# Optimization experiments

Hardware: AMD Instinct MI355X
Metric: run time of the kernel (lower is better)

## Reference

```python
import jax, jax.numpy as jnp
import numpy as np

N_EMBD = 1568  # 2 * 784, hard-coded in the source module
HEAD_SIZE = 128
BATCH = 16384


def setup_inputs() -> dict:
    key = jax.random.key(0)
    kx, kq, kk, kv = jax.random.split(key, 4)
    x = jax.random.normal(kx, (BATCH, N_EMBD), dtype=jnp.float32)
    wq = jax.random.normal(kq, (N_EMBD, HEAD_SIZE), dtype=jnp.float32) * (N_EMBD ** -0.5)
    wk = jax.random.normal(kk, (N_EMBD, HEAD_SIZE), dtype=jnp.float32) * (N_EMBD ** -0.5)
    wv = jax.random.normal(kv, (N_EMBD, HEAD_SIZE), dtype=jnp.float32) * (N_EMBD ** -0.5)
    return {"x": x, "wq": wq, "wk": wk, "wv": wv}


def reference(x, wq, wk, wv):
    # x: [B, N]; projections (bias-free Linear): [B, H]
    B, N = x.shape
    q = x @ wq
    k = x @ wk
    v = x @ wv
    # Outer-product score matrix per batch element: [B, H, H]
    attn = jnp.einsum('bi,bj->bij', q, k) * (N ** -0.5)  # scale uses FEATURE dim N, as in source
    attn = jax.nn.softmax(attn, axis=-1)
    # dropout is identity in eval mode
    out = jnp.einsum('bij,bj->bi', attn, v)  # [B, H]
    return out
```

## Files before the change

### kernel.cpp

```cpp
#include <hip/hip_runtime.h>
#include <stdint.h>

typedef unsigned short u16;
typedef __bf16 bf16x8 __attribute__((ext_vector_type(8)));
typedef float f32x4 __attribute__((ext_vector_type(4)));
typedef float f32x2 __attribute__((ext_vector_type(2)));

#define M_ROWS 16384
#define K_DIM  1568
#define H_DIM  128
#define NQ     384
#define MT     64
#define BK     32
#define NSTEP  49
#define NCH    8
#define CH_F   192
#define ASTR   200
#define TSTR   40
#define ABUF   (MT * ASTR)
#define PSTR   132
#define KSTRIDE (NQ * BK)
#define SCALE  0.02525381361380526f
#define LOG2E  1.4426950408889634f

__device__ __forceinline__ u16 f32_to_bf16_rne(float f) {
    uint32_t u = __float_as_uint(f);
    uint32_t r = (u + 0x7FFFu + ((u >> 16) & 1u)) >> 16;
    return (u16)r;
}

__device__ __forceinline__ uint32_t cvt_pk(float lo, float hi) {
    uint32_t d;
    asm("v_cvt_pk_bf16_f32 %0, %1, %2" : "=v"(d) : "v"(lo), "v"(hi));
    return d;
}

__device__ __forceinline__ f32x2 pk_mul(f32x2 a, f32x2 b) {
    f32x2 d; asm("v_pk_mul_f32 %0, %1, %2" : "=v"(d) : "v"(a), "v"(b)); return d;
}
__device__ __forceinline__ f32x2 pk_add(f32x2 a, f32x2 b) {
    f32x2 d; asm("v_pk_add_f32 %0, %1, %2" : "=v"(d) : "v"(a), "v"(b)); return d;
}
__device__ __forceinline__ f32x2 pk_fma(f32x2 a, f32x2 b, f32x2 c) {
    f32x2 d; asm("v_pk_fma_f32 %0, %1, %2, %3" : "=v"(d) : "v"(a), "v"(b), "v"(c)); return d;
}

__device__ __forceinline__ void cvt_wr8(u16* dst, f32x4 v) {
    uint2 t; t.x = cvt_pk(v.x, v.y); t.y = cvt_pk(v.z, v.w);
    *(uint2*)dst = t;
}

#define MFMA(a, b, c) __builtin_amdgcn_mfma_f32_16x16x32_bf16(a, b, c, 0, 0, 0)

__global__ __launch_bounds__(256) void wtrans_kernel(
    const float* __restrict__ wq, const float* __restrict__ wk,
    const float* __restrict__ wv, u16* __restrict__ wt2)
{
    __shared__ u16 tile[32][33];
    const float* w = (blockIdx.z == 0) ? wq : (blockIdx.z == 1) ? wk : wv;
    const int k0 = blockIdx.x * 32;
    const int nloc0 = blockIdx.y * 32;
    const int ng0 = blockIdx.z * 128 + nloc0;

    const int tn = threadIdx.x & 31;
    const int tk = threadIdx.x >> 5;
    #pragma unroll
    for (int p = 0; p < 4; p++) {
        int kk = tk + p * 8;
        tile[kk][tn] = f32_to_bf16_rne(w[(size_t)(k0 + kk) * H_DIM + nloc0 + tn]);
    }
    __syncthreads();

    const int klo = threadIdx.x & 31;
    const int tn2 = threadIdx.x >> 5;
    u16* dst = wt2 + (size_t)(k0 >> 5) * KSTRIDE;
    #pragma unroll
    for (int p = 0; p < 4; p++) {
        int nn = tn2 + p * 8;
        dst[(size_t)(ng0 + nn) * 32 + klo] = tile[klo][nn];
    }
}

__global__ __launch_bounds__(512, 2) void fused_kernel(
    const float* __restrict__ x,
    const u16* __restrict__ wt2,
    float* __restrict__ out)
{
    __shared__ char smem[3 * MT * PSTR * 4];
    u16* A0 = (u16*)smem;
    u16* A1 = A0 + ABUF;
    u16* TB = A1 + ABUF;
    float (*Pq)[PSTR] = (float (*)[PSTR])smem;
    float (*Pk)[PSTR] = (float (*)[PSTR])(smem + MT * PSTR * 4);
    float (*Pv)[PSTR] = (float (*)[PSTR])(smem + 2 * MT * PSTR * 4);

    const int tid  = threadIdx.x;
    const int lane = tid & 63;
    const int wave = tid >> 6;
    const int lrow = lane & 15;
    const int quad = lane >> 4;
    const int m0   = blockIdx.x * MT;

    const u16* bp0 = wt2 + (size_t)(wave * 48 +  0 + lrow) * 32 + quad * 8;
    const u16* bp1 = wt2 + (size_t)(wave * 48 + 16 + lrow) * 32 + quad * 8;
    const u16* bp2 = wt2 + (size_t)(wave * 48 + 32 + lrow) * 32 + quad * 8;

    const int srow = tid >> 3;
    const int st8  = tid & 7;
    const float* xrow = x + (size_t)(m0 + srow) * K_DIM;
    u16* wbs[2];
    wbs[0] = A0 + srow * ASTR + st8 * 4;
    wbs[1] = A1 + srow * ASTR + st8 * 4;

    const u16* aF[2][4];
    #pragma unroll
    for (int m = 0; m < 4; m++) {
        aF[0][m] = A0 + (m * 16 + lrow) * ASTR + quad * 8;
        aF[1][m] = A1 + (m * 16 + lrow) * ASTR + quad * 8;
    }

#define NTLD4(off) __builtin_nontemporal_load((const f32x4*)(xrow + (off)))
#define LOADC(S, OFF) do { \
    S[0] = NTLD4((OFF) + st8 * 4 +   0); \
    S[1] = NTLD4((OFF) + st8 * 4 +  32); \
    S[2] = NTLD4((OFF) + st8 * 4 +  64); \
    S[3] = NTLD4((OFF) + st8 * 4 +  96); \
    S[4] = NTLD4((OFF) + st8 * 4 + 128); \
    S[5] = NTLD4((OFF) + st8 * 4 + 160); \
} while (0)
#define WRITEC(WB, S) do { \
    cvt_wr8((WB) +   0, S[0]); cvt_wr8((WB) +  32, S[1]); \
    cvt_wr8((WB) +  64, S[2]); cvt_wr8((WB) +  96, S[3]); \
    cvt_wr8((WB) + 128, S[4]); cvt_wr8((WB) + 160, S[5]); \
} while (0)

    f32x4 acc00 = {}, acc01 = {}, acc02 = {};
    f32x4 acc10 = {}, acc11 = {}, acc12 = {};
    f32x4 acc20 = {}, acc21 = {}, acc22 = {};
    f32x4 acc30 = {}, acc31 = {}, acc32 = {};
    f32x4 sreg[2][6];

    LOADC(sreg[0], 0);
    f32x4 tl = NTLD4(1536 + st8 * 4);
    LOADC(sreg[1], CH_F);
    WRITEC(wbs[0], sreg[0]);
    cvt_wr8(TB + srow * TSTR + st8 * 4, tl);

    bf16x8 Ba0 = *(const bf16x8*)(bp0);
    bf16x8 Ba1 = *(const bf16x8*)(bp1);
    bf16x8 Ba2 = *(const bf16x8*)(bp2);
    bf16x8 Bb0 = *(const bf16x8*)(bp0 + KSTRIDE);
    bf16x8 Bb1 = *(const bf16x8*)(bp1 + KSTRIDE);
    bf16x8 Bb2 = *(const bf16x8*)(bp2 + KSTRIDE);
    __syncthreads();

#define KSTEP(AP, IT, G) do { \
    int gp = (G) + 2; if (gp > NSTEP - 1) gp = NSTEP - 1; \
    const size_t o = (size_t)gp * KSTRIDE; \
    bf16x8 Bc0 = *(const bf16x8*)(bp0 + o); \
    bf16x8 Bc1 = *(const bf16x8*)(bp1 + o); \
    bf16x8 Bc2 = *(const bf16x8*)(bp2 + o); \
    bf16x8 a0 = *(const bf16x8*)((AP)[0] + (IT) * BK); \
    bf16x8 a1 = *(const bf16x8*)((AP)[1] + (IT) * BK); \
    bf16x8 a2 = *(const bf16x8*)((AP)[2] + (IT) * BK); \
    bf16x8 a3 = *(const bf16x8*)((AP)[3] + (IT) * BK); \
    acc00 = MFMA(a0, Ba0, acc00); acc10 = MFMA(a1, Ba0, acc10); \
    acc20 = MFMA(a2, Ba0, acc20); acc30 = MFMA(a3, Ba0, acc30); \
    acc01 = MFMA(a0, Ba1, acc01); acc11 = MFMA(a1, Ba1, acc11); \
    acc21 = MFMA(a2, Ba1, acc21); acc31 = MFMA(a3, Ba1, acc31); \
    acc02 = MFMA(a0, Ba2, acc02); acc12 = MFMA(a1, Ba2, acc12); \
    acc22 = MFMA(a2, Ba2, acc22); acc32 = MFMA(a3, Ba2, acc32); \
    Ba0 = Bb0; Ba1 = Bb1; Ba2 = Bb2; Bb0 = Bc0; Bb1 = Bc1; Bb2 = Bc2; \
} while (0)

    #pragma unroll
    for (int c = 0; c < NCH; ++c) {
        if (c < NCH - 1) WRITEC(wbs[(c + 1) & 1], sreg[(c + 1) & 1]);
        if (c < NCH - 2) LOADC(sreg[c & 1], (c + 2) * CH_F);
        #pragma unroll
        for (int it = 0; it < 6; ++it) KSTEP(aF[c & 1], it, c * 6 + it);
        __syncthreads();
    }

    {
        bf16x8 a0 = *(const bf16x8*)(TB + (lrow +  0) * TSTR + quad * 8);
        bf16x8 a1 = *(const bf16x8*)(TB + (lrow + 16) * TSTR + quad * 8);
        bf16x8 a2 = *(const bf16x8*)(TB + (lrow + 32) * TSTR + quad * 8);
        bf16x8 a3 = *(const bf16x8*)(TB + (lrow + 48) * TSTR + quad * 8);
        acc00 = MFMA(a0, Ba0, acc00); acc10 = MFMA(a1, Ba0, acc10);
        acc20 = MFMA(a2, Ba0, acc20); acc30 = MFMA(a3, Ba0, acc30);
        acc01 = MFMA(a0, Ba1, acc01); acc11 = MFMA(a1, Ba1, acc11);
        acc21 = MFMA(a2, Ba1, acc21); acc31 = MFMA(a3, Ba1, acc31);
        acc02 = MFMA(a0, Ba2, acc02); acc12 = MFMA(a1, Ba2, acc12);
        acc22 = MFMA(a2, Ba2, acc22); acc32 = MFMA(a3, Ba2, acc32);
    }
    __syncthreads();

#define SCAT(ACC, MTi, NTi) do { \
    const int base = wave * 48 + (NTi) * 16; \
    const int sel  = base >> 7; \
    const int col  = (base & 127) + lrow; \
    const int mrow = (MTi) * 16 + quad * 4; \
    if (sel == 0)      { _Pragma("unroll") for (int rr = 0; rr < 4; rr++) Pq[mrow + rr][col] = ACC[rr] * (SCALE * LOG2E); } \
    else if (sel == 1) { _Pragma("unroll") for (int rr = 0; rr < 4; rr++) Pk[mrow + rr][col] = ACC[rr]; } \
    else               { _Pragma("unroll") for (int rr = 0; rr < 4; rr++) Pv[mrow + rr][col] = ACC[rr]; } \
} while (0)

    SCAT(acc00, 0, 0); SCAT(acc01, 0, 1); SCAT(acc02, 0, 2);
    SCAT(acc10, 1, 0); SCAT(acc11, 1, 1); SCAT(acc12, 1, 2);
    SCAT(acc20, 2, 0); SCAT(acc21, 2, 1); SCAT(acc22, 2, 2);
    SCAT(acc30, 3, 0); SCAT(acc31, 3, 1); SCAT(acc32, 3, 2);
    __syncthreads();

    const int r   = tid >> 3;
    const int sub = tid & 7;

    f32x4 qa = *(const f32x4*)&Pq[r][sub * 16 +  0];
    f32x4 qb = *(const f32x4*)&Pq[r][sub * 16 +  4];
    f32x4 qc = *(const f32x4*)&Pq[r][sub * 16 +  8];
    f32x4 qd = *(const f32x4*)&Pq[r][sub * 16 + 12];
    f32x2 qp0; qp0.x = qa.x; qp0.y = qa.y;
    f32x2 qp1; qp1.x = qa.z; qp1.y = qa.w;
    f32x2 qp2; qp2.x = qb.x; qp2.y = qb.y;
    f32x2 qp3; qp3.x = qb.z; qp3.y = qb.w;
    f32x2 qp4; qp4.x = qc.x; qp4.y = qc.y;
    f32x2 qp5; qp5.x = qc.z; qp5.y = qc.w;
    f32x2 qp6; qp6.x = qd.x; qp6.y = qd.y;
    f32x2 qp7; qp7.x = qd.z; qp7.y = qd.w;

    f32x2 d0 = {}, d1 = {}, d2 = {}, d3 = {}, d4 = {}, d5 = {}, d6 = {}, d7 = {};
    f32x2 n0 = {}, n1 = {}, n2 = {}, n3 = {}, n4 = {}, n5 = {}, n6 = {}, n7 = {};

    #pragma unroll 2
    for (int j4 = 0; j4 < 32; ++j4) {
        f32x4 k4 = *(const f32x4*)&Pk[r][j4 * 4];
        f32x4 v4 = *(const f32x4*)&Pv[r][j4 * 4];
        #pragma unroll
        for (int jj = 0; jj < 4; ++jj) {
            float kj = k4[jj];
            float vj = v4[jj];
            f32x2 kk; kk.x = kj; kk.y = kj;
            f32x2 vv; vv.x = vj; vv.y = vj;
            f32x2 s0 = pk_mul(qp0, kk);
            f32x2 s1 = pk_mul(qp1, kk);
            f32x2 s2 = pk_mul(qp2, kk);
            f32x2 s3 = pk_mul(qp3, kk);
            f32x2 s4 = pk_mul(qp4, kk);
            f32x2 s5 = pk_mul(qp5, kk);
            f32x2 s6 = pk_mul(qp6, kk);
            f32x2 s7 = pk_mul(qp7, kk);
            f32x2 e0; e0.x = __builtin_amdgcn_exp2f(s0.x); e0.y = __builtin_amdgcn_exp2f(s0.y);
            f32x2 e1; e1.x = __builtin_amdgcn_exp2f(s1.x); e1.y = __builtin_amdgcn_exp2f(s1.y);
            f32x2 e2; e2.x = __builtin_amdgcn_exp2f(s2.x); e2.y = __builtin_amdgcn_exp2f(s2.y);
            f32x2 e3; e3.x = __builtin_amdgcn_exp2f(s3.x); e3.y = __builtin_amdgcn_exp2f(s3.y);
            f32x2 e4; e4.x = __builtin_amdgcn_exp2f(s4.x); e4.y = __builtin_amdgcn_exp2f(s4.y);
            f32x2 e5; e5.x = __builtin_amdgcn_exp2f(s5.x); e5.y = __builtin_amdgcn_exp2f(s5.y);
            f32x2 e6; e6.x = __builtin_amdgcn_exp2f(s6.x); e6.y = __builtin_amdgcn_exp2f(s6.y);
            f32x2 e7; e7.x = __builtin_amdgcn_exp2f(s7.x); e7.y = __builtin_amdgcn_exp2f(s7.y);
            d0 = pk_add(d0, e0); n0 = pk_fma(e0, vv, n0);
            d1 = pk_add(d1, e1); n1 = pk_fma(e1, vv, n1);
            d2 = pk_add(d2, e2); n2 = pk_fma(e2, vv, n2);
            d3 = pk_add(d3, e3); n3 = pk_fma(e3, vv, n3);
            d4 = pk_add(d4, e4); n4 = pk_fma(e4, vv, n4);
            d5 = pk_add(d5, e5); n5 = pk_fma(e5, vv, n5);
            d6 = pk_add(d6, e6); n6 = pk_fma(e6, vv, n6);
            d7 = pk_add(d7, e7); n7 = pk_fma(e7, vv, n7);
        }
    }

    float* op = out + (size_t)(m0 + r) * H_DIM + sub * 16;
    f32x4 o0, o1, o2, o3;
    o0.x = n0.x / d0.x; o0.y = n0.y / d0.y; o0.z = n1.x / d1.x; o0.w = n1.y / d1.y;
    o1.x = n2.x / d2.x; o1.y = n2.y / d2.y; o1.z = n3.x / d3.x; o1.w = n3.y / d3.y;
    o2.x = n4.x / d4.x; o2.y = n4.y / d4.y; o2.z = n5.x / d5.x; o2.w = n5.y / d5.y;
    o3.x = n6.x / d6.x; o3.y = n6.y / d6.y; o3.z = n7.x / d7.x; o3.w = n7.y / d7.y;
    __builtin_nontemporal_store(o0, (f32x4*)(op +  0));
    __builtin_nontemporal_store(o1, (f32x4*)(op +  4));
    __builtin_nontemporal_store(o2, (f32x4*)(op +  8));
    __builtin_nontemporal_store(o3, (f32x4*)(op + 12));
}

extern "C" void kernel_launch(void* const* d_in, const int* in_sizes, int n_in,
                              void* d_out, int out_size, void* d_ws, size_t ws_size,
                              hipStream_t stream)
{
    const float* x  = (const float*)d_in[0];
    const float* wq = (const float*)d_in[1];
    const float* wk = (const float*)d_in[2];
    const float* wv = (const float*)d_in[3];
    float* out = (float*)d_out;

    u16* wt2 = (u16*)d_ws;

    wtrans_kernel<<<dim3(K_DIM / 32, H_DIM / 32, 3), 256, 0, stream>>>(wq, wk, wv, wt2);
    fused_kernel<<<M_ROWS / MT, 512, 0, stream>>>(x, wt2, out);
}
```

Measured before the change: 195.9 us.

## Split fused projection+attention into separate GEMM and attention kernels via workspace

When the workspace is large enough, the fused kernel is replaced by a projection kernel that writes scaled Q/K/V (fp32) to global memory, followed by a separate attention kernel that does the per-row outer-product softmax with 16 rows per 256-thread block. The aim is to lift the LDS footprint and occupancy limit that the fused epilogue imposes on the GEMM, and to spread the attention work over more threads. In exchange it adds a 25 MB write and read of the projection buffer and an extra launch. The old fused path is kept as a fallback.

Result: slower. 207.6 us (+6.0%).

```diff
diff --git a/kernel.cpp b/kernel.cpp
--- a/kernel.cpp
+++ b/kernel.cpp
@@ -23,6 +23,8 @@
 #define SCALE  0.02525381361380526f
 #define LOG2E  1.4426950408889634f
 
+#define WS_NEEDED ((size_t)M_ROWS * NQ * 4 + (size_t)NSTEP * KSTRIDE * 2)
+
 __device__ __forceinline__ u16 f32_to_bf16_rne(float f) {
     uint32_t u = __float_as_uint(f);
     uint32_t r = (u + 0x7FFFu + ((u >> 16) & 1u)) >> 16;
@@ -81,42 +83,27 @@
     }
 }
 
-__global__ __launch_bounds__(512, 2) void fused_kernel(
-    const float* __restrict__ x,
-    const u16* __restrict__ wt2,
-    float* __restrict__ out)
-{
-    __shared__ char smem[3 * MT * PSTR * 4];
-    u16* A0 = (u16*)smem;
-    u16* A1 = A0 + ABUF;
-    u16* TB = A1 + ABUF;
-    float (*Pq)[PSTR] = (float (*)[PSTR])smem;
-    float (*Pk)[PSTR] = (float (*)[PSTR])(smem + MT * PSTR * 4);
-    float (*Pv)[PSTR] = (float (*)[PSTR])(smem + 2 * MT * PSTR * 4);
-
-    const int tid  = threadIdx.x;
-    const int lane = tid & 63;
-    const int wave = tid >> 6;
-    const int lrow = lane & 15;
-    const int quad = lane >> 4;
-    const int m0   = blockIdx.x * MT;
-
-    const u16* bp0 = wt2 + (size_t)(wave * 48 +  0 + lrow) * 32 + quad * 8;
-    const u16* bp1 = wt2 + (size_t)(wave * 48 + 16 + lrow) * 32 + quad * 8;
-    const u16* bp2 = wt2 + (size_t)(wave * 48 + 32 + lrow) * 32 + quad * 8;
-
-    const int srow = tid >> 3;
-    const int st8  = tid & 7;
-    const float* xrow = x + (size_t)(m0 + srow) * K_DIM;
-    u16* wbs[2];
-    wbs[0] = A0 + srow * ASTR + st8 * 4;
-    wbs[1] = A1 + srow * ASTR + st8 * 4;
-
-    const u16* aF[2][4];
-    #pragma unroll
-    for (int m = 0; m < 4; m++) {
-        aF[0][m] = A0 + (m * 16 + lrow) * ASTR + quad * 8;
-        aF[1][m] = A1 + (m * 16 + lrow) * ASTR + quad * 8;
+#define GEMM_BODY_DECLS \
+    const int tid  = threadIdx.x; \
+    const int lane = tid & 63; \
+    const int wave = tid >> 6; \
+    const int lrow = lane & 15; \
+    const int quad = lane >> 4; \
+    const int m0   = blockIdx.x * MT; \
+    const u16* bp0 = wt2 + (size_t)(wave * 48 +  0 + lrow) * 32 + quad * 8; \
+    const u16* bp1 = wt2 + (size_t)(wave * 48 + 16 + lrow) * 32 + quad * 8; \
+    const u16* bp2 = wt2 + (size_t)(wave * 48 + 32 + lrow) * 32 + quad * 8; \
+    const int srow = tid >> 3; \
+    const int st8  = tid & 7; \
+    const float* xrow = x + (size_t)(m0 + srow) * K_DIM; \
+    u16* wbs[2]; \
+    wbs[0] = A0 + srow * ASTR + st8 * 4; \
+    wbs[1] = A1 + srow * ASTR + st8 * 4; \
+    const u16* aF[2][4]; \
+    _Pragma("unroll") \
+    for (int m = 0; m < 4; m++) { \
+        aF[0][m] = A0 + (m * 16 + lrow) * ASTR + quad * 8; \
+        aF[1][m] = A1 + (m * 16 + lrow) * ASTR + quad * 8; \
     }
 
 #define NTLD4(off) __builtin_nontemporal_load((const f32x4*)(xrow + (off)))
@@ -133,26 +120,6 @@
     cvt_wr8((WB) +  64, S[2]); cvt_wr8((WB) +  96, S[3]); \
     cvt_wr8((WB) + 128, S[4]); cvt_wr8((WB) + 160, S[5]); \
 } while (0)
-
-    f32x4 acc00 = {}, acc01 = {}, acc02 = {};
-    f32x4 acc10 = {}, acc11 = {}, acc12 = {};
-    f32x4 acc20 = {}, acc21 = {}, acc22 = {};
-    f32x4 acc30 = {}, acc31 = {}, acc32 = {};
-    f32x4 sreg[2][6];
-
-    LOADC(sreg[0], 0);
-    f32x4 tl = NTLD4(1536 + st8 * 4);
-    LOADC(sreg[1], CH_F);
-    WRITEC(wbs[0], sreg[0]);
-    cvt_wr8(TB + srow * TSTR + st8 * 4, tl);
-
-    bf16x8 Ba0 = *(const bf16x8*)(bp0);
-    bf16x8 Ba1 = *(const bf16x8*)(bp1);
-    bf16x8 Ba2 = *(const bf16x8*)(bp2);
-    bf16x8 Bb0 = *(const bf16x8*)(bp0 + KSTRIDE);
-    bf16x8 Bb1 = *(const bf16x8*)(bp1 + KSTRIDE);
-    bf16x8 Bb2 = *(const bf16x8*)(bp2 + KSTRIDE);
-    __syncthreads();
 
 #define KSTEP(AP, IT, G) do { \
     int gp = (G) + 2; if (gp > NSTEP - 1) gp = NSTEP - 1; \
@@ -173,27 +140,85 @@
     Ba0 = Bb0; Ba1 = Bb1; Ba2 = Bb2; Bb0 = Bc0; Bb1 = Bc1; Bb2 = Bc2; \
 } while (0)
 
-    #pragma unroll
-    for (int c = 0; c < NCH; ++c) {
-        if (c < NCH - 1) WRITEC(wbs[(c + 1) & 1], sreg[(c + 1) & 1]);
-        if (c < NCH - 2) LOADC(sreg[c & 1], (c + 2) * CH_F);
-        #pragma unroll
-        for (int it = 0; it < 6; ++it) KSTEP(aF[c & 1], it, c * 6 + it);
-        __syncthreads();
-    }
-
-    {
-        bf16x8 a0 = *(const bf16x8*)(TB + (lrow +  0) * TSTR + quad * 8);
-        bf16x8 a1 = *(const bf16x8*)(TB + (lrow + 16) * TSTR + quad * 8);
-        bf16x8 a2 = *(const bf16x8*)(TB + (lrow + 32) * TSTR + quad * 8);
-        bf16x8 a3 = *(const bf16x8*)(TB + (lrow + 48) * TSTR + quad * 8);
-        acc00 = MFMA(a0, Ba0, acc00); acc10 = MFMA(a1, Ba0, acc10);
-        acc20 = MFMA(a2, Ba0, acc20); acc30 = MFMA(a3, Ba0, acc30);
-        acc01 = MFMA(a0, Ba1, acc01); acc11 = MFMA(a1, Ba1, acc11);
-        acc21 = MFMA(a2, Ba1, acc21); acc31 = MFMA(a3, Ba1, acc31);
-        acc02 = MFMA(a0, Ba2, acc02); acc12 = MFMA(a1, Ba2, acc12);
-        acc22 = MFMA(a2, Ba2, acc22); acc32 = MFMA(a3, Ba2, acc32);
-    }
+#define GEMM_MAIN \
+    f32x4 acc00 = {}, acc01 = {}, acc02 = {}; \
+    f32x4 acc10 = {}, acc11 = {}, acc12 = {}; \
+    f32x4 acc20 = {}, acc21 = {}, acc22 = {}; \
+    f32x4 acc30 = {}, acc31 = {}, acc32 = {}; \
+    f32x4 sreg[2][6]; \
+    LOADC(sreg[0], 0); \
+    f32x4 tl = NTLD4(1536 + st8 * 4); \
+    LOADC(sreg[1], CH_F); \
+    WRITEC(wbs[0], sreg[0]); \
+    cvt_wr8(TB + srow * TSTR + st8 * 4, tl); \
+    bf16x8 Ba0 = *(const bf16x8*)(bp0); \
+    bf16x8 Ba1 = *(const bf16x8*)(bp1); \
+    bf16x8 Ba2 = *(const bf16x8*)(bp2); \
+    bf16x8 Bb0 = *(const bf16x8*)(bp0 + KSTRIDE); \
+    bf16x8 Bb1 = *(const bf16x8*)(bp1 + KSTRIDE); \
+    bf16x8 Bb2 = *(const bf16x8*)(bp2 + KSTRIDE); \
+    __syncthreads(); \
+    _Pragma("unroll") \
+    for (int c = 0; c < NCH; ++c) { \
+        if (c < NCH - 1) WRITEC(wbs[(c + 1) & 1], sreg[(c + 1) & 1]); \
+        if (c < NCH - 2) LOADC(sreg[c & 1], (c + 2) * CH_F); \
+        _Pragma("unroll") \
+        for (int it = 0; it < 6; ++it) KSTEP(aF[c & 1], it, c * 6 + it); \
+        __syncthreads(); \
+    } \
+    { \
+        bf16x8 a0 = *(const bf16x8*)(TB + (lrow +  0) * TSTR + quad * 8); \
+        bf16x8 a1 = *(const bf16x8*)(TB + (lrow + 16) * TSTR + quad * 8); \
+        bf16x8 a2 = *(const bf16x8*)(TB + (lrow + 32) * TSTR + quad * 8); \
+        bf16x8 a3 = *(const bf16x8*)(TB + (lrow + 48) * TSTR + quad * 8); \
+        acc00 = MFMA(a0, Ba0, acc00); acc10 = MFMA(a1, Ba0, acc10); \
+        acc20 = MFMA(a2, Ba0, acc20); acc30 = MFMA(a3, Ba0, acc30); \
+        acc01 = MFMA(a0, Ba1, acc01); acc11 = MFMA(a1, Ba1, acc11); \
+        acc21 = MFMA(a2, Ba1, acc21); acc31 = MFMA(a3, Ba1, acc31); \
+        acc02 = MFMA(a0, Ba2, acc02); acc12 = MFMA(a1, Ba2, acc12); \
+        acc22 = MFMA(a2, Ba2, acc22); acc32 = MFMA(a3, Ba2, acc32); \
+    }
+
+__global__ __launch_bounds__(512, 2) void proj_kernel(
+    const float* __restrict__ x, const u16* __restrict__ wt2,
+    float* __restrict__ P)
+{
+    __shared__ char smem[2 * ABUF * 2 + MT * TSTR * 2];
+    u16* A0 = (u16*)smem;
+    u16* A1 = A0 + ABUF;
+    u16* TB = A1 + ABUF;
+
+    GEMM_BODY_DECLS
+    GEMM_MAIN
+
+#define SCATG(ACC, MTi, NTi) do { \
+    const int n   = wave * 48 + (NTi) * 16 + lrow; \
+    const float sc = (n < 128) ? (SCALE * LOG2E) : 1.0f; \
+    const int mrow = m0 + (MTi) * 16 + quad * 4; \
+    _Pragma("unroll") for (int rr = 0; rr < 4; rr++) \
+        __builtin_nontemporal_store(ACC[rr] * sc, &P[(size_t)(mrow + rr) * NQ + n]); \
+} while (0)
+
+    SCATG(acc00, 0, 0); SCATG(acc01, 0, 1); SCATG(acc02, 0, 2);
+    SCATG(acc10, 1, 0); SCATG(acc11, 1, 1); SCATG(acc12, 1, 2);
+    SCATG(acc20, 2, 0); SCATG(acc21, 2, 1); SCATG(acc22, 2, 2);
+    SCATG(acc30, 3, 0); SCATG(acc31, 3, 1); SCATG(acc32, 3, 2);
+}
+
+__global__ __launch_bounds__(512, 2) void fused_kernel(
+    const float* __restrict__ x, const u16* __restrict__ wt2,
+    float* __restrict__ out)
+{
+    __shared__ char smem[3 * MT * PSTR * 4];
+    u16* A0 = (u16*)smem;
+    u16* A1 = A0 + ABUF;
+    u16* TB = A1 + ABUF;
+    float (*Pq)[PSTR] = (float (*)[PSTR])smem;
+    float (*Pk)[PSTR] = (float (*)[PSTR])(smem + MT * PSTR * 4);
+    float (*Pv)[PSTR] = (float (*)[PSTR])(smem + 2 * MT * PSTR * 4);
+
+    GEMM_BODY_DECLS
+    GEMM_MAIN
     __syncthreads();
 
 #define SCAT(ACC, MTi, NTi) do { \
@@ -280,6 +305,59 @@
     __builtin_nontemporal_store(o3, (f32x4*)(op + 12));
 }
 
+__global__ __launch_bounds__(256) void attn_kernel(
+    const float* __restrict__ P,
+    float* __restrict__ out)
+{
+    const int tid  = threadIdx.x;
+    const int rloc = tid >> 4;
+    const int sub  = tid & 15;
+    const int row  = blockIdx.x * 16 + rloc;
+    const float* pr = P + (size_t)row * NQ;
+
+    f32x4 qa = *(const f32x4*)(pr + sub * 8);
+    f32x4 qb = *(const f32x4*)(pr + sub * 8 + 4);
+    f32x2 qp0; qp0.x = qa.x; qp0.y = qa.y;
+    f32x2 qp1; qp1.x = qa.z; qp1.y = qa.w;
+    f32x2 qp2; qp2.x = qb.x; qp2.y = qb.y;
+    f32x2 qp3; qp3.x = qb.z; qp3.y = qb.w;
+
+    f32x2 d0 = {}, d1 = {}, d2 = {}, d3 = {};
+    f32x2 n0 = {}, n1 = {}, n2 = {}, n3 = {};
+
+    #pragma unroll 4
+    for (int j4 = 0; j4 < 32; ++j4) {
+        f32x4 k4 = *(const f32x4*)(pr + 128 + j4 * 4);
+        f32x4 v4 = *(const f32x4*)(pr + 256 + j4 * 4);
+        #pragma unroll
+        for (int jj = 0; jj < 4; ++jj) {
+            float kj = k4[jj];
+            float vj = v4[jj];
+            f32x2 kk; kk.x = kj; kk.y = kj;
+            f32x2 vv; vv.x = vj; vv.y = vj;
+            f32x2 s0 = pk_mul(qp0, kk);
+            f32x2 s1 = pk_mul(qp1, kk);
+            f32x2 s2 = pk_mul(qp2, kk);
+            f32x2 s3 = pk_mul(qp3, kk);
+            f32x2 e0; e0.x = __builtin_amdgcn_exp2f(s0.x); e0.y = __builtin_amdgcn_exp2f(s0.y);
+            f32x2 e1; e1.x = __builtin_amdgcn_exp2f(s1.x); e1.y = __builtin_amdgcn_exp2f(s1.y);
+            f32x2 e2; e2.x = __builtin_amdgcn_exp2f(s2.x); e2.y = __builtin_amdgcn_exp2f(s2.y);
+            f32x2 e3; e3.x = __builtin_amdgcn_exp2f(s3.x); e3.y = __builtin_amdgcn_exp2f(s3.y);
+            d0 = pk_add(d0, e0); n0 = pk_fma(e0, vv, n0);
+            d1 = pk_add(d1, e1); n1 = pk_fma(e1, vv, n1);
+            d2 = pk_add(d2, e2); n2 = pk_fma(e2, vv, n2);
+            d3 = pk_add(d3, e3); n3 = pk_fma(e3, vv, n3);
+        }
+    }
+
+    float* op = out + (size_t)row * H_DIM + sub * 8;
+    f32x4 o0, o1;
+    o0.x = n0.x / d0.x; o0.y = n0.y / d0.y; o0.z = n1.x / d1.x; o0.w = n1.y / d1.y;
+    o1.x = n2.x / d2.x; o1.y = n2.y / d2.y; o1.z = n3.x / d3.x; o1.w = n3.y / d3.y;
+    __builtin_nontemporal_store(o0, (f32x4*)(op));
+    __builtin_nontemporal_store(o1, (f32x4*)(op + 4));
+}
+
 extern "C" void kernel_launch(void* const* d_in, const int* in_sizes, int n_in,
                               void* d_out, int out_size, void* d_ws, size_t ws_size,
                               hipStream_t stream)
@@ -290,8 +368,15 @@
     const float* wv = (const float*)d_in[3];
     float* out = (float*)d_out;
 
-    u16* wt2 = (u16*)d_ws;
-
-    wtrans_kernel<<<dim3(K_DIM / 32, H_DIM / 32, 3), 256, 0, stream>>>(wq, wk, wv, wt2);
-    fused_kernel<<<M_ROWS / MT, 512, 0, stream>>>(x, wt2, out);
-}
+    if (ws_size >= WS_NEEDED) {
+        float* P   = (float*)d_ws;
+        u16*   wt2 = (u16*)((char*)d_ws + (size_t)M_ROWS * NQ * 4);
+        wtrans_kernel<<<dim3(K_DIM / 32, H_DIM / 32, 3), 256, 0, stream>>>(wq, wk, wv, wt2);
+        proj_kernel<<<M_ROWS / MT, 512, 0, stream>>>(x, wt2, P);
+        attn_kernel<<<M_ROWS / 16, 256, 0, stream>>>(P, out);
+    } else {
+        u16* wt2 = (u16*)d_ws;
+        wtrans_kernel<<<dim3(K_DIM / 32, H_DIM / 32, 3), 256, 0, stream>>>(wq, wk, wv, wt2);
+        fused_kernel<<<M_ROWS / MT, 512, 0, stream>>>(x, wt2, out);
+    }
+}
```

## Halve row tile to 32 and raise occupancy to four blocks per CU

Applied to the files above, without the earlier changes.

Shrinks the per-block row tile from 64 to 32 rows, which halves the MFMA accumulators and softmax registers per thread and lets launch bounds request four blocks per CU. The x staging now has 16 threads per row, each loading 12 contiguous floats with regular loads instead of nontemporal ones. The weight prefetch is deepened from two to three k-steps ahead. The aim is more latency hiding through occupancy, at the cost of each block loading the full weight slice for half as many rows, which doubles weight traffic from L2.

Result: slower. 205.2 us (+4.8%).

```diff
diff --git a/kernel.cpp b/kernel.cpp
--- a/kernel.cpp
+++ b/kernel.cpp
@@ -10,10 +10,11 @@
 #define K_DIM  1568
 #define H_DIM  128
 #define NQ     384
-#define MT     64
+#define MT     32
 #define BK     32
 #define NSTEP  49
 #define NCH    8
+#define CHK    6
 #define CH_F   192
 #define ASTR   200
 #define TSTR   40
@@ -81,7 +82,7 @@
     }
 }
 
-__global__ __launch_bounds__(512, 2) void fused_kernel(
+__global__ __launch_bounds__(512, 4) void fused_kernel(
     const float* __restrict__ x,
     const u16* __restrict__ wt2,
     float* __restrict__ out)
@@ -105,46 +106,39 @@
     const u16* bp1 = wt2 + (size_t)(wave * 48 + 16 + lrow) * 32 + quad * 8;
     const u16* bp2 = wt2 + (size_t)(wave * 48 + 32 + lrow) * 32 + quad * 8;
 
-    const int srow = tid >> 3;
-    const int st8  = tid & 7;
+    const int srow = tid >> 4;
+    const int st16 = tid & 15;
     const float* xrow = x + (size_t)(m0 + srow) * K_DIM;
     u16* wbs[2];
-    wbs[0] = A0 + srow * ASTR + st8 * 4;
-    wbs[1] = A1 + srow * ASTR + st8 * 4;
-
-    const u16* aF[2][4];
-    #pragma unroll
-    for (int m = 0; m < 4; m++) {
+    wbs[0] = A0 + srow * ASTR + st16 * 12;
+    wbs[1] = A1 + srow * ASTR + st16 * 12;
+
+    const u16* aF[2][2];
+    #pragma unroll
+    for (int m = 0; m < 2; m++) {
         aF[0][m] = A0 + (m * 16 + lrow) * ASTR + quad * 8;
         aF[1][m] = A1 + (m * 16 + lrow) * ASTR + quad * 8;
     }
 
-#define NTLD4(off) __builtin_nontemporal_load((const f32x4*)(xrow + (off)))
+#define LD4(off) (*(const f32x4*)(xrow + (off)))
 #define LOADC(S, OFF) do { \
-    S[0] = NTLD4((OFF) + st8 * 4 +   0); \
-    S[1] = NTLD4((OFF) + st8 * 4 +  32); \
-    S[2] = NTLD4((OFF) + st8 * 4 +  64); \
-    S[3] = NTLD4((OFF) + st8 * 4 +  96); \
-    S[4] = NTLD4((OFF) + st8 * 4 + 128); \
-    S[5] = NTLD4((OFF) + st8 * 4 + 160); \
+    S[0] = LD4((OFF) + st16 * 12 + 0); \
+    S[1] = LD4((OFF) + st16 * 12 + 4); \
+    S[2] = LD4((OFF) + st16 * 12 + 8); \
 } while (0)
 #define WRITEC(WB, S) do { \
-    cvt_wr8((WB) +   0, S[0]); cvt_wr8((WB) +  32, S[1]); \
-    cvt_wr8((WB) +  64, S[2]); cvt_wr8((WB) +  96, S[3]); \
-    cvt_wr8((WB) + 128, S[4]); cvt_wr8((WB) + 160, S[5]); \
+    cvt_wr8((WB) + 0, S[0]); cvt_wr8((WB) + 4, S[1]); cvt_wr8((WB) + 8, S[2]); \
 } while (0)
 
     f32x4 acc00 = {}, acc01 = {}, acc02 = {};
     f32x4 acc10 = {}, acc11 = {}, acc12 = {};
-    f32x4 acc20 = {}, acc21 = {}, acc22 = {};
-    f32x4 acc30 = {}, acc31 = {}, acc32 = {};
-    f32x4 sreg[2][6];
+    f32x4 sreg[2][3];
 
     LOADC(sreg[0], 0);
-    f32x4 tl = NTLD4(1536 + st8 * 4);
+    f32x2 tl = *(const f32x2*)(xrow + 1536 + st16 * 2);
     LOADC(sreg[1], CH_F);
     WRITEC(wbs[0], sreg[0]);
-    cvt_wr8(TB + srow * TSTR + st8 * 4, tl);
+    *(uint32_t*)(TB + srow * TSTR + st16 * 2) = cvt_pk(tl.x, tl.y);
 
     bf16x8 Ba0 = *(const bf16x8*)(bp0);
     bf16x8 Ba1 = *(const bf16x8*)(bp1);
@@ -152,25 +146,25 @@
     bf16x8 Bb0 = *(const bf16x8*)(bp0 + KSTRIDE);
     bf16x8 Bb1 = *(const bf16x8*)(bp1 + KSTRIDE);
     bf16x8 Bb2 = *(const bf16x8*)(bp2 + KSTRIDE);
+    bf16x8 Bc0 = *(const bf16x8*)(bp0 + 2 * KSTRIDE);
+    bf16x8 Bc1 = *(const bf16x8*)(bp1 + 2 * KSTRIDE);
+    bf16x8 Bc2 = *(const bf16x8*)(bp2 + 2 * KSTRIDE);
     __syncthreads();
 
 #define KSTEP(AP, IT, G) do { \
-    int gp = (G) + 2; if (gp > NSTEP - 1) gp = NSTEP - 1; \
+    int gp = (G) + 3; if (gp > NSTEP - 1) gp = NSTEP - 1; \
     const size_t o = (size_t)gp * KSTRIDE; \
-    bf16x8 Bc0 = *(const bf16x8*)(bp0 + o); \
-    bf16x8 Bc1 = *(const bf16x8*)(bp1 + o); \
-    bf16x8 Bc2 = *(const bf16x8*)(bp2 + o); \
+    bf16x8 Bd0 = *(const bf16x8*)(bp0 + o); \
+    bf16x8 Bd1 = *(const bf16x8*)(bp1 + o); \
+    bf16x8 Bd2 = *(const bf16x8*)(bp2 + o); \
     bf16x8 a0 = *(const bf16x8*)((AP)[0] + (IT) * BK); \
     bf16x8 a1 = *(const bf16x8*)((AP)[1] + (IT) * BK); \
-    bf16x8 a2 = *(const bf16x8*)((AP)[2] + (IT) * BK); \
-    bf16x8 a3 = *(const bf16x8*)((AP)[3] + (IT) * BK); \
     acc00 = MFMA(a0, Ba0, acc00); acc10 = MFMA(a1, Ba0, acc10); \
-    acc20 = MFMA(a2, Ba0, acc20); acc30 = MFMA(a3, Ba0, acc30); \
     acc01 = MFMA(a0, Ba1, acc01); acc11 = MFMA(a1, Ba1, acc11); \
-    acc21 = MFMA(a2, Ba1, acc21); acc31 = MFMA(a3, Ba1, acc31); \
     acc02 = MFMA(a0, Ba2, acc02); acc12 = MFMA(a1, Ba2, acc12); \
-    acc22 = MFMA(a2, Ba2, acc22); acc32 = MFMA(a3, Ba2, acc32); \
-    Ba0 = Bb0; Ba1 = Bb1; Ba2 = Bb2; Bb0 = Bc0; Bb1 = Bc1; Bb2 = Bc2; \
+    Ba0 = Bb0; Ba1 = Bb1; Ba2 = Bb2; \
+    Bb0 = Bc0; Bb1 = Bc1; Bb2 = Bc2; \
+    Bc0 = Bd0; Bc1 = Bd1; Bc2 = Bd2; \
 } while (0)
 
     #pragma unroll
@@ -178,21 +172,16 @@
         if (c < NCH - 1) WRITEC(wbs[(c + 1) & 1], sreg[(c + 1) & 1]);
         if (c < NCH - 2) LOADC(sreg[c & 1], (c + 2) * CH_F);
         #pragma unroll
-        for (int it = 0; it < 6; ++it) KSTEP(aF[c & 1], it, c * 6 + it);
+        for (int it = 0; it < CHK; ++it) KSTEP(aF[c & 1], it, c * CHK + it);
         __syncthreads();
     }
 
     {
         bf16x8 a0 = *(const bf16x8*)(TB + (lrow +  0) * TSTR + quad * 8);
         bf16x8 a1 = *(const bf16x8*)(TB + (lrow + 16) * TSTR + quad * 8);
-        bf16x8 a2 = *(const bf16x8*)(TB + (lrow + 32) * TSTR + quad * 8);
-        bf16x8 a3 = *(const bf16x8*)(TB + (lrow + 48) * TSTR + quad * 8);
         acc00 = MFMA(a0, Ba0, acc00); acc10 = MFMA(a1, Ba0, acc10);
-        acc20 = MFMA(a2, Ba0, acc20); acc30 = MFMA(a3, Ba0, acc30);
         acc01 = MFMA(a0, Ba1, acc01); acc11 = MFMA(a1, Ba1, acc11);
-        acc21 = MFMA(a2, Ba1, acc21); acc31 = MFMA(a3, Ba1, acc31);
         acc02 = MFMA(a0, Ba2, acc02); acc12 = MFMA(a1, Ba2, acc12);
-        acc22 = MFMA(a2, Ba2, acc22); acc32 = MFMA(a3, Ba2, acc32);
     }
     __syncthreads();
 
@@ -208,30 +197,22 @@
 
     SCAT(acc00, 0, 0); SCAT(acc01, 0, 1); SCAT(acc02, 0, 2);
     SCAT(acc10, 1, 0); SCAT(acc11, 1, 1); SCAT(acc12, 1, 2);
-    SCAT(acc20, 2, 0); SCAT(acc21, 2, 1); SCAT(acc22, 2, 2);
-    SCAT(acc30, 3, 0); SCAT(acc31, 3, 1); SCAT(acc32, 3, 2);
-    __syncthreads();
-
-    const int r   = tid >> 3;
-    const int sub = tid & 7;
-
-    f32x4 qa = *(const f32x4*)&Pq[r][sub * 16 +  0];
-    f32x4 qb = *(const f32x4*)&Pq[r][sub * 16 +  4];
-    f32x4 qc = *(const f32x4*)&Pq[r][sub * 16 +  8];
-    f32x4 qd = *(const f32x4*)&Pq[r][sub * 16 + 12];
+    __syncthreads();
+
+    const int r   = tid >> 4;
+    const int sub = tid & 15;
+
+    f32x4 qa = *(const f32x4*)&Pq[r][sub * 8];
+    f32x4 qb = *(const f32x4*)&Pq[r][sub * 8 + 4];
     f32x2 qp0; qp0.x = qa.x; qp0.y = qa.y;
     f32x2 qp1; qp1.x = qa.z; qp1.y = qa.w;
     f32x2 qp2; qp2.x = qb.x; qp2.y = qb.y;
     f32x2 qp3; qp3.x = qb.z; qp3.y = qb.w;
-    f32x2 qp4; qp4.x = qc.x; qp4.y = qc.y;
-    f32x2 qp5; qp5.x = qc.z; qp5.y = qc.w;
-    f32x2 qp6; qp6.x = qd.x; qp6.y = qd.y;
-    f32x2 qp7; qp7.x = qd.z; qp7.y = qd.w;
-
-    f32x2 d0 = {}, d1 = {}, d2 = {}, d3 = {}, d4 = {}, d5 = {}, d6 = {}, d7 = {};
-    f32x2 n0 = {}, n1 = {}, n2 = {}, n3 = {}, n4 = {}, n5 = {}, n6 = {}, n7 = {};
-
-    #pragma unroll 2
+
+    f32x2 d0 = {}, d1 = {}, d2 = {}, d3 = {};
+    f32x2 n0 = {}, n1 = {}, n2 = {}, n3 = {};
+
+    #pragma unroll 4
     for (int j4 = 0; j4 < 32; ++j4) {
         f32x4 k4 = *(const f32x4*)&Pk[r][j4 * 4];
         f32x4 v4 = *(const f32x4*)&Pv[r][j4 * 4];
@@ -245,39 +226,23 @@
             f32x2 s1 = pk_mul(qp1, kk);
             f32x2 s2 = pk_mul(qp2, kk);
             f32x2 s3 = pk_mul(qp3, kk);
-            f32x2 s4 = pk_mul(qp4, kk);
-            f32x2 s5 = pk_mul(qp5, kk);
-            f32x2 s6 = pk_mul(qp6, kk);
-            f32x2 s7 = pk_mul(qp7, kk);
             f32x2 e0; e0.x = __builtin_amdgcn_exp2f(s0.x); e0.y = __builtin_amdgcn_exp2f(s0.y);
             f32x2 e1; e1.x = __builtin_amdgcn_exp2f(s1.x); e1.y = __builtin_amdgcn_exp2f(s1.y);
             f32x2 e2; e2.x = __builtin_amdgcn_exp2f(s2.x); e2.y = __builtin_amdgcn_exp2f(s2.y);
             f32x2 e3; e3.x = __builtin_amdgcn_exp2f(s3.x); e3.y = __builtin_amdgcn_exp2f(s3.y);
-            f32x2 e4; e4.x = __builtin_amdgcn_exp2f(s4.x); e4.y = __builtin_amdgcn_exp2f(s4.y);
-            f32x2 e5; e5.x = __builtin_amdgcn_exp2f(s5.x); e5.y = __builtin_amdgcn_exp2f(s5.y);
-            f32x2 e6; e6.x = __builtin_amdgcn_exp2f(s6.x); e6.y = __builtin_amdgcn_exp2f(s6.y);
-            f32x2 e7; e7.x = __builtin_amdgcn_exp2f(s7.x); e7.y = __builtin_amdgcn_exp2f(s7.y);
             d0 = pk_add(d0, e0); n0 = pk_fma(e0, vv, n0);
             d1 = pk_add(d1, e1); n1 = pk_fma(e1, vv, n1);
             d2 = pk_add(d2, e2); n2 = pk_fma(e2, vv, n2);
             d3 = pk_add(d3, e3); n3 = pk_fma(e3, vv, n3);
-            d4 = pk_add(d4, e4); n4 = pk_fma(e4, vv, n4);
-            d5 = pk_add(d5, e5); n5 = pk_fma(e5, vv, n5);
-            d6 = pk_add(d6, e6); n6 = pk_fma(e6, vv, n6);
-            d7 = pk_add(d7, e7); n7 = pk_fma(e7, vv, n7);
         }
     }
 
-    float* op = out + (size_t)(m0 + r) * H_DIM + sub * 16;
-    f32x4 o0, o1, o2, o3;
+    float* op = out + (size_t)(m0 + r) * H_DIM + sub * 8;
+    f32x4 o0, o1;
     o0.x = n0.x / d0.x; o0.y = n0.y / d0.y; o0.z = n1.x / d1.x; o0.w = n1.y / d1.y;
     o1.x = n2.x / d2.x; o1.y = n2.y / d2.y; o1.z = n3.x / d3.x; o1.w = n3.y / d3.y;
-    o2.x = n4.x / d4.x; o2.y = n4.y / d4.y; o2.z = n5.x / d5.x; o2.w = n5.y / d5.y;
-    o3.x = n6.x / d6.x; o3.y = n6.y / d6.y; o3.z = n7.x / d7.x; o3.w = n7.y / d7.y;
-    __builtin_nontemporal_store(o0, (f32x4*)(op +  0));
-    __builtin_nontemporal_store(o1, (f32x4*)(op +  4));
-    __builtin_nontemporal_store(o2, (f32x4*)(op +  8));
-    __builtin_nontemporal_store(o3, (f32x4*)(op + 12));
+    __builtin_nontemporal_store(o0, (f32x4*)(op));
+    __builtin_nontemporal_store(o1, (f32x4*)(op + 4));
 }
 
 extern "C" void kernel_launch(void* const* d_in, const int* in_sizes, int n_in,
```
